# Kernel tuning notes

Measured on AMD Instinct MI355X. Metric: run time of the kernel, lower is better.

The kernel has to match this reference:

```python
import jax, jax.numpy as jnp
import numpy as np
import math

B, S, D_EMB = 1, 4096, 768
N_HEADS, D_QKV = 12, 64
INV_TEMP = 1.0


def setup_inputs() -> dict:
    key = jax.random.key(0)
    ks = jax.random.split(key, 11)
    s = 0.02
    return {
        "q_in": jax.random.normal(ks[0], (B, S, D_EMB), jnp.float32),
        "k_in": jax.random.normal(ks[1], (B, S, D_EMB), jnp.float32),
        "v_in": jax.random.normal(ks[2], (B, S, D_EMB), jnp.float32),
        "W_q": jax.random.normal(ks[3], (D_EMB, N_HEADS * D_QKV), jnp.float32) * s,
        "b_q": jnp.zeros((N_HEADS * D_QKV,), jnp.float32),
        "W_k": jax.random.normal(ks[4], (D_EMB, N_HEADS * D_QKV), jnp.float32) * s,
        "b_k": jnp.zeros((N_HEADS * D_QKV,), jnp.float32),
        "W_v": jax.random.normal(ks[5], (D_EMB, N_HEADS * D_QKV), jnp.float32) * s,
        "b_v": jnp.zeros((N_HEADS * D_QKV,), jnp.float32),
        "W_o": jax.random.normal(ks[6], (N_HEADS * D_QKV, D_EMB), jnp.float32) * s,
        "b_o": jnp.zeros((D_EMB,), jnp.float32),
    }


def _split_heads(x):  # [B,S,H*D] -> [B,H,S,D]
    b, s, _ = x.shape
    return x.reshape(b, s, N_HEADS, D_QKV).transpose(0, 2, 1, 3)


def reference(q_in, k_in, v_in, W_q, b_q, W_k, b_k, W_v, b_v, W_o, b_o):
    q = _split_heads(q_in @ W_q + b_q)
    k = _split_heads(k_in @ W_k + b_k)
    v = _split_heads(v_in @ W_v + b_v)
    # full [B,H,S,S] score matrix (module materializes it for custom masking)
    scores = INV_TEMP * jnp.einsum('bhqd,bhkd->bhqk', q, k) / math.sqrt(D_QKV)
    attn = jax.nn.softmax(scores, axis=-1)
    out = jnp.einsum('bhqk,bhkd->bhqd', attn, v)  # [B,H,S,D]
    out = out.transpose(0, 2, 1, 3).reshape(q_in.shape[0], q_in.shape[1], N_HEADS * D_QKV)
    return out @ W_o + b_o
```

## Files before the change

### kernel.cpp

```cpp
#include <hip/hip_runtime.h>

#define S 4096
#define E 768
#define NH 12
#define DH 64
#define QSCALE (0.125f * 1.44269504f)
#define KSPLIT 4

typedef __bf16 bf16;
typedef __bf16 bf16x4 __attribute__((ext_vector_type(4)));
typedef __bf16 bf16x8 __attribute__((ext_vector_type(8)));
typedef float  f32x4  __attribute__((ext_vector_type(4)));

#define MFMA(a, b, c) __builtin_amdgcn_mfma_f32_16x16x32_bf16(a, b, c, 0, 0, 0)

__device__ __forceinline__ void async16(const bf16* g, bf16* l) {
  __builtin_amdgcn_global_load_lds(
      (const __attribute__((address_space(1))) void*)g,
      (__attribute__((address_space(3))) void*)l, 16, 0, 0);
}

__global__ __launch_bounds__(256) void prologue(const float* __restrict__ q_in,
                                                const float* __restrict__ k_in,
                                                const float* __restrict__ v_in,
                                                const float* __restrict__ w0,
                                                const float* __restrict__ w1,
                                                const float* __restrict__ w2,
                                                const float* __restrict__ w3,
                                                bf16* __restrict__ qb,
                                                bf16* __restrict__ kb,
                                                bf16* __restrict__ vb,
                                                bf16* __restrict__ t0,
                                                bf16* __restrict__ t1,
                                                bf16* __restrict__ t2,
                                                bf16* __restrict__ t3) {
  const int bid = blockIdx.x, tid = threadIdx.x;
  if (bid < 2304) {
    const int z = bid / 576, rem = bid % 576;
    const int bx = rem % 24, by = rem / 24;
    const float* W = z == 0 ? w0 : (z == 1 ? w1 : (z == 2 ? w2 : w3));
    bf16* Wt = z == 0 ? t0 : (z == 1 ? t1 : (z == 2 ? t2 : t3));
    __shared__ float t[32][33];
    const int tx = tid & 31, ty = tid >> 5;
    for (int j = ty; j < 32; j += 8)
      t[j][tx] = W[(by * 32 + j) * E + bx * 32 + tx];
    __syncthreads();
    for (int j = ty; j < 32; j += 8)
      Wt[(bx * 32 + j) * E + by * 32 + tx] = (bf16)t[tx][j];
  } else {
    const int b2 = bid - 2304;
    const int z = b2 / 3072, r2 = b2 % 3072;
    const float* in = z == 0 ? q_in : (z == 1 ? k_in : v_in);
    bf16* out = z == 0 ? qb : (z == 1 ? kb : vb);
    const int i = r2 * 1024 + tid * 4;
    float4 v = *(const float4*)(in + i);
    bf16x4 o = { (bf16)v.x, (bf16)v.y, (bf16)v.z, (bf16)v.w };
    *(bf16x4*)(out + i) = o;
  }
}

__global__ __launch_bounds__(256) void gemm128(const bf16* __restrict__ A0,
                                               const bf16* __restrict__ A1,
                                               const bf16* __restrict__ A2,
                                               const bf16* __restrict__ B0,
                                               const bf16* __restrict__ B1,
                                               const bf16* __restrict__ B2,
                                               const float* __restrict__ bias0,
                                               const float* __restrict__ bias1,
                                               const float* __restrict__ bias2,
                                               bf16* __restrict__ C0,
                                               bf16* __restrict__ C1,
                                               bf16* __restrict__ C2) {
  __shared__ __align__(16) bf16 smem[128 * 136];
  bf16* Asm = smem;
  bf16* Bsm = smem + 4096;
  bf16* Cs  = smem;

  const int z = blockIdx.z;
  const bf16* A  = z == 0 ? A0 : (z == 1 ? A1 : A2);
  const bf16* Bt = z == 0 ? B0 : (z == 1 ? B1 : B2);
  const float* bias = z == 0 ? bias0 : (z == 1 ? bias1 : bias2);

  const int tid = threadIdx.x;
  const int wv = tid >> 6, lane = tid & 63;
  const int quad = lane >> 4, l16 = lane & 15;
  const int m0 = blockIdx.x * 128, n0 = blockIdx.y * 128;
  const int wm = (wv >> 1) * 64, wn = (wv & 1) * 64;
  const int srow = lane >> 2, scol = (lane & 3) * 8;

  f32x4 acc[4][4] = {};

  for (int k0 = 0; k0 < E; k0 += 32) {
#pragma unroll
    for (int j = 0; j < 2; j++) {
      const int ch = wv * 2 + j;
      async16(&A[(size_t)(m0 + ch * 16 + srow) * E + k0 + scol], &Asm[ch * 512]);
      async16(&Bt[(size_t)(n0 + ch * 16 + srow) * E + k0 + scol], &Bsm[ch * 512]);
    }
    __syncthreads();
    bf16x8 af[4], bfv[4];
#pragma unroll
    for (int mi = 0; mi < 4; mi++)
      af[mi] = *(const bf16x8*)&Asm[(wm + mi * 16 + l16) * 32 + quad * 8];
#pragma unroll
    for (int ni = 0; ni < 4; ni++)
      bfv[ni] = *(const bf16x8*)&Bsm[(wn + ni * 16 + l16) * 32 + quad * 8];
#pragma unroll
    for (int mi = 0; mi < 4; mi++)
#pragma unroll
      for (int ni = 0; ni < 4; ni++)
        acc[mi][ni] = MFMA(af[mi], bfv[ni], acc[mi][ni]);
    __syncthreads();
  }

  const float scale = (z == 0) ? QSCALE : 1.0f;
#pragma unroll
  for (int mi = 0; mi < 4; mi++) {
#pragma unroll
    for (int ni = 0; ni < 4; ni++) {
      const int nl = wn + ni * 16 + l16;
      const float bv = bias[n0 + nl];
#pragma unroll
      for (int r = 0; r < 4; r++) {
        const int ml = wm + mi * 16 + quad * 4 + r;
        const float v = (acc[mi][ni][r] + bv) * scale;
        if (z == 2) Cs[nl * 136 + ml] = (bf16)v;
        else        Cs[ml * 136 + nl] = (bf16)v;
      }
    }
  }
  __syncthreads();

  if (z == 0) {
    const int e = lane & 7;
#pragma unroll
    for (int p = 0; p < 8; p++) {
      const int hr = p * 32 + wv * 8 + (lane >> 3);
      const int r = hr >> 1, hf = hr & 1;
      bf16x8 c = *(const bf16x8*)&Cs[r * 136 + hf * 64 + e * 8];
      *(bf16x8*)(C0 + (size_t)((n0 >> 6) + hf) * S * DH + (size_t)(m0 + r) * DH + e * 8) = c;
    }
  } else {
    bf16* dst = (z == 1) ? C1 : C2;
#pragma unroll
    for (int p = 0; p < 8; p++) {
      const int cid = p * 4 + wv;
      const int reg = cid >> 3;
      const int i = cid & 7;
      const int h_l = reg >> 1, tile = reg & 1;
      bf16x8 c;
      if (z == 1) {
        const int row = tile * 64 + (i >> 1) * 16 + l16;
        const int col = h_l * 64 + (i & 1) * 32 + quad * 8;
        c = *(const bf16x8*)&Cs[row * 136 + col];
      } else {
        const int nl = h_l * 64 + (i >> 1) * 16 + l16;
        const int ml = tile * 64 + (i & 1) * 32 + quad * 8;
        c = *(const bf16x8*)&Cs[nl * 136 + ml];
      }
      *(bf16x8*)(dst + (size_t)((n0 >> 6) + h_l) * S * DH +
                 (size_t)((m0 >> 6) + tile) * 4096 + i * 512 + lane * 8) = c;
    }
  }
}

__global__ __launch_bounds__(256, 3) void attn(const bf16* __restrict__ Q,
                                               const bf16* __restrict__ Kf,
                                               const bf16* __restrict__ Vf,
                                               bf16* __restrict__ Op0,
                                               bf16* __restrict__ Op1,
                                               bf16* __restrict__ Op2,
                                               bf16* __restrict__ Op3,
                                               float* __restrict__ Lp) {
  __shared__ bf16 P[4][64][68];
  const int h = blockIdx.y, ks = blockIdx.z;
  const int tid = threadIdx.x;
  const int wave = tid >> 6, lane = tid & 63;
  const int quad = lane >> 4, l16 = lane & 15;
  const int q0 = blockIdx.x * 256 + wave * 64;

  const bf16* Qh = Q + (size_t)h * S * DH;
  const bf16* kbase = Kf + (size_t)h * S * DH + (size_t)ks * (S / KSPLIT) * DH + lane * 8;
  const bf16* vbase = Vf + (size_t)h * S * DH + (size_t)ks * (S / KSPLIT) * DH + lane * 8;
  bf16* Op = ks == 0 ? Op0 : (ks == 1 ? Op1 : (ks == 2 ? Op2 : Op3));

  bf16x8 aq[4][2];
#pragma unroll
  for (int mi = 0; mi < 4; mi++)
#pragma unroll
    for (int j = 0; j < 2; j++)
      aq[mi][j] = *(const bf16x8*)&Qh[(size_t)(q0 + mi * 16 + l16) * DH + j * 32 + quad * 8];

  bf16x8 ones;
#pragma unroll
  for (int e = 0; e < 8; e++) ones[e] = (bf16)1.0f;

  f32x4 o[4][4] = {};
  f32x4 ol[4] = {};

  const int T = (S / KSPLIT) / 64;
  for (int t = 0; t < T; ++t) {
    const bf16* kp = kbase + (size_t)t * 4096;
    bf16x8 kr[8];
#pragma unroll
    for (int i = 0; i < 8; i++) kr[i] = *(const bf16x8*)(kp + i * 512);

#pragma unroll
    for (int mi = 0; mi < 4; mi++) {
      f32x4 sfr[4] = {};
#pragma unroll
      for (int nb = 0; nb < 4; nb++) {
        sfr[nb] = MFMA(aq[mi][0], kr[nb * 2], sfr[nb]);
        sfr[nb] = MFMA(aq[mi][1], kr[nb * 2 + 1], sfr[nb]);
      }
#pragma unroll
      for (int nb = 0; nb < 4; nb++)
#pragma unroll
        for (int r = 0; r < 4; r++)
          P[wave][mi * 16 + quad * 4 + r][nb * 16 + l16] = (bf16)__builtin_exp2f(sfr[nb][r]);
    }

    bf16x8 ap[4][2];
#pragma unroll
    for (int mi = 0; mi < 4; mi++)
#pragma unroll
      for (int j = 0; j < 2; j++)
        ap[mi][j] = *(const bf16x8*)&P[wave][mi * 16 + l16][j * 32 + quad * 8];

#pragma unroll
    for (int mi = 0; mi < 4; mi++) {
      ol[mi] = MFMA(ap[mi][0], ones, ol[mi]);
      ol[mi] = MFMA(ap[mi][1], ones, ol[mi]);
    }

    const bf16* vp = vbase + (size_t)t * 4096;
#pragma unroll
    for (int db = 0; db < 4; db++) {
      bf16x8 v0 = *(const bf16x8*)(vp + (db * 2) * 512);
      bf16x8 v1 = *(const bf16x8*)(vp + (db * 2 + 1) * 512);
#pragma unroll
      for (int mi = 0; mi < 4; mi++) {
        o[db][mi] = MFMA(ap[mi][0], v0, o[db][mi]);
        o[db][mi] = MFMA(ap[mi][1], v1, o[db][mi]);
      }
    }
  }

  float* Lph = Lp + (size_t)(ks * NH + h) * S;
  if (l16 == 0) {
#pragma unroll
    for (int mi = 0; mi < 4; mi++)
#pragma unroll
      for (int r = 0; r < 4; r++)
        Lph[q0 + mi * 16 + quad * 4 + r] = ol[mi][r];
  }
#pragma unroll
  for (int db = 0; db < 4; db++) {
    const int d = db * 16 + l16;
#pragma unroll
    for (int mi = 0; mi < 4; mi++)
#pragma unroll
      for (int r = 0; r < 4; r++) {
        const int row = q0 + mi * 16 + quad * 4 + r;
        Op[(size_t)row * E + h * DH + d] = (bf16)o[db][mi][r];
      }
  }
}

__global__ __launch_bounds__(256) void combine(const bf16* __restrict__ Op0,
                                               const bf16* __restrict__ Op1,
                                               const bf16* __restrict__ Op2,
                                               const bf16* __restrict__ Op3,
                                               const float* __restrict__ Lp,
                                               bf16* __restrict__ Obf) {
  const int i8 = blockIdx.x * 256 + threadIdx.x;
  const size_t base = (size_t)i8 * 8;
  const int row = (int)(base / E), c = (int)(base % E);
  const int h = c >> 6;
  const float l = Lp[(size_t)h * S + row] + Lp[(size_t)(NH + h) * S + row] +
                  Lp[(size_t)(2 * NH + h) * S + row] + Lp[(size_t)(3 * NH + h) * S + row];
  const float rl = 1.0f / l;
  bf16x8 a = *(const bf16x8*)(Op0 + base);
  bf16x8 b = *(const bf16x8*)(Op1 + base);
  bf16x8 cc = *(const bf16x8*)(Op2 + base);
  bf16x8 d = *(const bf16x8*)(Op3 + base);
  bf16x8 o;
#pragma unroll
  for (int e = 0; e < 8; e++)
    o[e] = (bf16)((((float)a[e] + (float)b[e]) + ((float)cc[e] + (float)d[e])) * rl);
  *(bf16x8*)(Obf + base) = o;
}

__global__ __launch_bounds__(256) void gemm64(const bf16* __restrict__ A,
                                              const bf16* __restrict__ Bt,
                                              const float* __restrict__ bias,
                                              float* __restrict__ C) {
  __shared__ __align__(16) bf16 Asm[64 * 32];
  __shared__ __align__(16) bf16 Bsm[64 * 32];
  const int tid = threadIdx.x;
  const int wv = tid >> 6, lane = tid & 63;
  const int quad = lane >> 4, l16 = lane & 15;
  const int m0 = blockIdx.x * 64, n0 = blockIdx.y * 64;
  const int srow = lane >> 2, scol = (lane & 3) * 8;

  f32x4 acc[4] = {};

  for (int k0 = 0; k0 < E; k0 += 32) {
    async16(&A[(size_t)(m0 + wv * 16 + srow) * E + k0 + scol], &Asm[wv * 512]);
    async16(&Bt[(size_t)(n0 + wv * 16 + srow) * E + k0 + scol], &Bsm[wv * 512]);
    __syncthreads();
    bf16x8 af = *(const bf16x8*)&Asm[(wv * 16 + l16) * 32 + quad * 8];
#pragma unroll
    for (int ni = 0; ni < 4; ni++) {
      bf16x8 bfr = *(const bf16x8*)&Bsm[(ni * 16 + l16) * 32 + quad * 8];
      acc[ni] = MFMA(af, bfr, acc[ni]);
    }
    __syncthreads();
  }

  const int row0 = m0 + wv * 16 + quad * 4;
#pragma unroll
  for (int ni = 0; ni < 4; ni++) {
    const int col = n0 + ni * 16 + l16;
    const float bv = bias[col];
#pragma unroll
    for (int r = 0; r < 4; r++)
      C[(size_t)(row0 + r) * E + col] = acc[ni][r] + bv;
  }
}

extern "C" void kernel_launch(void* const* d_in, const int* in_sizes, int n_in,
                              void* d_out, int out_size, void* d_ws, size_t ws_size,
                              hipStream_t stream) {
  (void)in_sizes; (void)n_in; (void)out_size; (void)ws_size;
  const float* q_in = (const float*)d_in[0];
  const float* k_in = (const float*)d_in[1];
  const float* v_in = (const float*)d_in[2];
  const float* W_q  = (const float*)d_in[3];
  const float* b_q  = (const float*)d_in[4];
  const float* W_k  = (const float*)d_in[5];
  const float* b_k  = (const float*)d_in[6];
  const float* W_v  = (const float*)d_in[7];
  const float* b_v  = (const float*)d_in[8];
  const float* W_o  = (const float*)d_in[9];
  const float* b_o  = (const float*)d_in[10];

  const size_t SE2 = (size_t)S * E * 2;
  const size_t EE2 = (size_t)E * E * 2;
  char* ws = (char*)d_ws;
  bf16* qb  = (bf16*)(ws);
  bf16* kb  = (bf16*)(ws + SE2);
  bf16* vb  = (bf16*)(ws + 2 * SE2);
  bf16* WqT = (bf16*)(ws + 3 * SE2);
  bf16* WkT = (bf16*)(ws + 3 * SE2 + EE2);
  bf16* WvT = (bf16*)(ws + 3 * SE2 + 2 * EE2);
  bf16* WoT = (bf16*)(ws + 3 * SE2 + 3 * EE2);
  bf16* Qh  = (bf16*)(ws + 3 * SE2 + 4 * EE2);
  bf16* Kf  = (bf16*)(ws + 4 * SE2 + 4 * EE2);
  bf16* Vf  = (bf16*)(ws + 5 * SE2 + 4 * EE2);
  bf16* Obf = (bf16*)(ws + 6 * SE2 + 4 * EE2);
  bf16* Op1 = qb;
  bf16* Op2 = kb;
  bf16* Op3 = vb;
  float* Lp = (float*)WqT;

  prologue<<<dim3(2304 + 3 * 3072), 256, 0, stream>>>(
      q_in, k_in, v_in, W_q, W_k, W_v, W_o, qb, kb, vb, WqT, WkT, WvT, WoT);

  gemm128<<<dim3(S / 128, E / 128, 3), 256, 0, stream>>>(
      qb, kb, vb, WqT, WkT, WvT, b_q, b_k, b_v, Qh, Kf, Vf);

  attn<<<dim3(S / 256, NH, KSPLIT), 256, 0, stream>>>(Qh, Kf, Vf, Obf, Op1, Op2, Op3, Lp);

  combine<<<dim3(S * E / 2048), 256, 0, stream>>>(Obf, Op1, Op2, Op3, Lp, Obf);

  gemm64<<<dim3(S / 64, E / 64), 256, 0, stream>>>(Obf, WoT, b_o, (float*)d_out);
}
```

Before: 236.1 us.

## Transpose attention MFMA operands, vectorize P stores and output via LDS, widen gemm K-step

The attention kernel now computes S^T by swapping MFMA operands. Each lane can then write four consecutive exp values as one bf16x4 store into a padded, 16-byte aligned LDS tile (row stride 72), replacing scalar scattered stores. The output tile is also staged through LDS so global writes become coalesced 16-byte stores instead of scalar bf16 scatters. The output projection gemm loads two 32-wide K chunks per barrier pair, halving the synchronization count at the cost of more shared memory.

```diff
diff --git a/kernel.cpp b/kernel.cpp
--- a/kernel.cpp
+++ b/kernel.cpp
@@ -172,7 +172,7 @@
                                                bf16* __restrict__ Op2,
                                                bf16* __restrict__ Op3,
                                                float* __restrict__ Lp) {
-  __shared__ bf16 P[4][64][68];
+  __shared__ __align__(16) bf16 P2[4][64][72];
   const int h = blockIdx.y, ks = blockIdx.z;
   const int tid = threadIdx.x;
   const int wave = tid >> 6, lane = tid & 63;
@@ -186,10 +186,10 @@
 
   bf16x8 aq[4][2];
 #pragma unroll
-  for (int mi = 0; mi < 4; mi++)
+  for (int qb = 0; qb < 4; qb++)
 #pragma unroll
     for (int j = 0; j < 2; j++)
-      aq[mi][j] = *(const bf16x8*)&Qh[(size_t)(q0 + mi * 16 + l16) * DH + j * 32 + quad * 8];
+      aq[qb][j] = *(const bf16x8*)&Qh[(size_t)(q0 + qb * 16 + l16) * DH + j * 32 + quad * 8];
 
   bf16x8 ones;
 #pragma unroll
@@ -197,6 +197,8 @@
 
   f32x4 o[4][4] = {};
   f32x4 ol[4] = {};
+
+  bf16* Pw = &P2[wave][0][0];
 
   const int T = (S / KSPLIT) / 64;
   for (int t = 0; t < T; ++t) {
@@ -206,31 +208,29 @@
     for (int i = 0; i < 8; i++) kr[i] = *(const bf16x8*)(kp + i * 512);
 
 #pragma unroll
-    for (int mi = 0; mi < 4; mi++) {
-      f32x4 sfr[4] = {};
-#pragma unroll
-      for (int nb = 0; nb < 4; nb++) {
-        sfr[nb] = MFMA(aq[mi][0], kr[nb * 2], sfr[nb]);
-        sfr[nb] = MFMA(aq[mi][1], kr[nb * 2 + 1], sfr[nb]);
-      }
-#pragma unroll
-      for (int nb = 0; nb < 4; nb++)
-#pragma unroll
-        for (int r = 0; r < 4; r++)
-          P[wave][mi * 16 + quad * 4 + r][nb * 16 + l16] = (bf16)__builtin_exp2f(sfr[nb][r]);
-    }
-
-    bf16x8 ap[4][2];
-#pragma unroll
-    for (int mi = 0; mi < 4; mi++)
-#pragma unroll
-      for (int j = 0; j < 2; j++)
-        ap[mi][j] = *(const bf16x8*)&P[wave][mi * 16 + l16][j * 32 + quad * 8];
-
-#pragma unroll
-    for (int mi = 0; mi < 4; mi++) {
-      ol[mi] = MFMA(ap[mi][0], ones, ol[mi]);
-      ol[mi] = MFMA(ap[mi][1], ones, ol[mi]);
+    for (int kb = 0; kb < 4; kb++)
+#pragma unroll
+      for (int qb = 0; qb < 4; qb++) {
+        f32x4 st = {};
+        st = MFMA(kr[kb * 2], aq[qb][0], st);
+        st = MFMA(kr[kb * 2 + 1], aq[qb][1], st);
+        bf16x4 pk;
+#pragma unroll
+        for (int r = 0; r < 4; r++) pk[r] = (bf16)__builtin_exp2f(st[r]);
+        *(bf16x4*)&Pw[(qb * 16 + l16) * 72 + kb * 16 + quad * 4] = pk;
+      }
+
+    bf16x8 bp[4][2];
+#pragma unroll
+    for (int qb = 0; qb < 4; qb++)
+#pragma unroll
+      for (int jc = 0; jc < 2; jc++)
+        bp[qb][jc] = *(const bf16x8*)&Pw[(qb * 16 + l16) * 72 + jc * 32 + quad * 8];
+
+#pragma unroll
+    for (int qb = 0; qb < 4; qb++) {
+      ol[qb] = MFMA(ones, bp[qb][0], ol[qb]);
+      ol[qb] = MFMA(ones, bp[qb][1], ol[qb]);
     }
 
     const bf16* vp = vbase + (size_t)t * 4096;
@@ -239,31 +239,36 @@
       bf16x8 v0 = *(const bf16x8*)(vp + (db * 2) * 512);
       bf16x8 v1 = *(const bf16x8*)(vp + (db * 2 + 1) * 512);
 #pragma unroll
-      for (int mi = 0; mi < 4; mi++) {
-        o[db][mi] = MFMA(ap[mi][0], v0, o[db][mi]);
-        o[db][mi] = MFMA(ap[mi][1], v1, o[db][mi]);
+      for (int qb = 0; qb < 4; qb++) {
+        o[db][qb] = MFMA(v0, bp[qb][0], o[db][qb]);
+        o[db][qb] = MFMA(v1, bp[qb][1], o[db][qb]);
       }
     }
   }
 
   float* Lph = Lp + (size_t)(ks * NH + h) * S;
-  if (l16 == 0) {
-#pragma unroll
-    for (int mi = 0; mi < 4; mi++)
-#pragma unroll
-      for (int r = 0; r < 4; r++)
-        Lph[q0 + mi * 16 + quad * 4 + r] = ol[mi][r];
-  }
-#pragma unroll
-  for (int db = 0; db < 4; db++) {
-    const int d = db * 16 + l16;
-#pragma unroll
-    for (int mi = 0; mi < 4; mi++)
-#pragma unroll
-      for (int r = 0; r < 4; r++) {
-        const int row = q0 + mi * 16 + quad * 4 + r;
-        Op[(size_t)row * E + h * DH + d] = (bf16)o[db][mi][r];
-      }
+  if (quad == 0) {
+#pragma unroll
+    for (int qb = 0; qb < 4; qb++)
+      Lph[q0 + qb * 16 + l16] = ol[qb][0];
+  }
+#pragma unroll
+  for (int db = 0; db < 4; db++)
+#pragma unroll
+    for (int qb = 0; qb < 4; qb++) {
+      bf16x4 pk;
+#pragma unroll
+      for (int r = 0; r < 4; r++) pk[r] = (bf16)o[db][qb][r];
+      *(bf16x4*)&Pw[(qb * 16 + l16) * 72 + db * 16 + quad * 4] = pk;
+    }
+  {
+    const int rr = lane >> 3, ee = (lane & 7) * 8;
+#pragma unroll
+    for (int p = 0; p < 8; p++) {
+      const int row = p * 8 + rr;
+      bf16x8 c = *(const bf16x8*)&Pw[row * 72 + ee];
+      *(bf16x8*)(Op + (size_t)(q0 + row) * E + h * DH + ee) = c;
+    }
   }
 }
 
@@ -295,8 +300,8 @@
                                               const bf16* __restrict__ Bt,
                                               const float* __restrict__ bias,
                                               float* __restrict__ C) {
-  __shared__ __align__(16) bf16 Asm[64 * 32];
-  __shared__ __align__(16) bf16 Bsm[64 * 32];
+  __shared__ __align__(16) bf16 Asm[2][64 * 32];
+  __shared__ __align__(16) bf16 Bsm[2][64 * 32];
   const int tid = threadIdx.x;
   const int wv = tid >> 6, lane = tid & 63;
   const int quad = lane >> 4, l16 = lane & 15;
@@ -305,15 +310,21 @@
 
   f32x4 acc[4] = {};
 
-  for (int k0 = 0; k0 < E; k0 += 32) {
-    async16(&A[(size_t)(m0 + wv * 16 + srow) * E + k0 + scol], &Asm[wv * 512]);
-    async16(&Bt[(size_t)(n0 + wv * 16 + srow) * E + k0 + scol], &Bsm[wv * 512]);
-    __syncthreads();
-    bf16x8 af = *(const bf16x8*)&Asm[(wv * 16 + l16) * 32 + quad * 8];
-#pragma unroll
-    for (int ni = 0; ni < 4; ni++) {
-      bf16x8 bfr = *(const bf16x8*)&Bsm[(ni * 16 + l16) * 32 + quad * 8];
-      acc[ni] = MFMA(af, bfr, acc[ni]);
+  for (int k0 = 0; k0 < E; k0 += 64) {
+#pragma unroll
+    for (int jc = 0; jc < 2; jc++) {
+      async16(&A[(size_t)(m0 + wv * 16 + srow) * E + k0 + jc * 32 + scol], &Asm[jc][wv * 512]);
+      async16(&Bt[(size_t)(n0 + wv * 16 + srow) * E + k0 + jc * 32 + scol], &Bsm[jc][wv * 512]);
+    }
+    __syncthreads();
+#pragma unroll
+    for (int jc = 0; jc < 2; jc++) {
+      bf16x8 af = *(const bf16x8*)&Asm[jc][(wv * 16 + l16) * 32 + quad * 8];
+#pragma unroll
+      for (int ni = 0; ni < 4; ni++) {
+        bf16x8 bfr = *(const bf16x8*)&Bsm[jc][(ni * 16 + l16) * 32 + quad * 8];
+        acc[ni] = MFMA(af, bfr, acc[ni]);
+      }
     }
     __syncthreads();
   }
```

Measured after the change: 227.4 us. 3.7% less time.
